# Optimization experiments

Measured on AMD Instinct MI355X. Metric: run time of the kernel, lower is better.

Reference implementation:

```python
import jax, jax.numpy as jnp
import numpy as np

# Central-difference gradients on a 5D field (b, d1, d2, d3, c); slices crop
# the two non-differentiated spatial axes by 1 on each side so all outputs align.

def grad_dx(f):
    return (f[:, 2:, 1:-1, 1:-1] - f[:, :-2, 1:-1, 1:-1]) * 0.5

def grad_dy(f):
    return (f[:, 1:-1, 2:, 1:-1] - f[:, 1:-1, :-2, 1:-1]) * 0.5

def grad_dz(f):
    return (f[:, 1:-1, 1:-1, 2:] - f[:, 1:-1, 1:-1, :-2]) * 0.5


def setup_inputs() -> dict:
    key = jax.random.key(0)
    ddf = jax.random.normal(key, (4, 160, 160, 160, 3), dtype=jnp.float32)
    return {"ddf": ddf}


def reference(ddf) -> jnp.ndarray:
    # first derivatives: (b, d-2, h-2, w-2, 3)
    dfdx = grad_dx(ddf)
    dfdy = grad_dy(ddf)
    dfdz = grad_dz(ddf)
    # second derivatives: (b, d-4, h-4, w-4, 3)
    dfdxx = grad_dx(dfdx)
    dfdyy = grad_dy(dfdy)
    dfdzz = grad_dz(dfdz)
    dfdxy = grad_dy(dfdx)
    dfdyz = grad_dz(dfdy)
    dfdxz = grad_dz(dfdx)
    energy = (dfdxx ** 2 + dfdyy ** 2 + dfdzz ** 2
              + 2.0 * dfdxy ** 2 + 2.0 * dfdxz ** 2 + 2.0 * dfdyz ** 2)
    return jnp.mean(energy, axis=(1, 2, 3, 4))  # shape (batch,)
```

## Files before the change

kernel.cpp:

```cpp
#include <hip/hip_runtime.h>


typedef float F4 __attribute__((ext_vector_type(4)));

#define DIM 160
#define SX (DIM * DIM * 3)
#define SY (DIM * 3)
#define FSZ ((long long)DIM * SX)
#define TOT (4LL * FSZ)

#define ROWS 20
#define ROWU 37
#define USED_U (ROWS * ROWU)
#define SLICE_U 744
#define SLICE_F (SLICE_U * 4)
#define SLOTS 4
#define STEPS 26
#define NSEG 6
#define NMS 4
#define NYT 10
#define NBLK (4 * NSEG * NMS * NYT)
#define CPX (NBLK / 8)

#define CB(a, i) a[(i) >> 2][(i) & 3]

__global__ __launch_bounds__(256, 2) void be_kernel(const float* __restrict__ f,
                                                    float* __restrict__ out) {
    __shared__ float lds[SLICE_F * SLOTS];
    const int tid = threadIdx.x;

    int lid = (blockIdx.x & 7) * CPX + (blockIdx.x >> 3);
    int p2i = lid / (NMS * NYT);
    int q2i = lid % (NMS * NYT);
    int b = p2i / NSEG, xseg = p2i % NSEG;
    int ms = q2i / NYT, yt = q2i % NYT;

    const int X0 = 2 + xseg * STEPS;
    const int gy0 = 16 * yt;
    const int core = 4 + 128 * ms;
    const int Gm = core - 8;
    const long long bb = (long long)b * FSZ;
    const float* fbase = f + bb;
    const float* fend = f + (TOT - 4);

    const int t = tid >> 4;
    const int yy = tid & 15;
    const int m0 = core + 8 * t;
    const int y = 2 + 16 * yt + yy;

    int jlo = 6 - m0; if (jlo < 0) jlo = 0;
    int jhi = 474 - m0; if (jhi > 8) jhi = 8;
    if (y >= DIM - 2) jhi = -1;

    const int rc = (yy + 2) * ROWU + 2 * t;

    long long choff[3];
#pragma unroll
    for (int it = 0; it < 3; ++it) {
        int c = it * 256 + tid;
        int row = c / ROWU, col = c - row * ROWU;
        choff[it] = (long long)(gy0 + row) * SY + Gm + 4 * col;
    }
    const bool ch2ok = (512 + tid) < USED_U;

    auto stage = [&](int slab, int slot) {
        long long sb = (long long)slab * SX;
#pragma unroll
        for (int it = 0; it < 3; ++it) {
            if (it < 2 || ch2ok) {
                const float* gp = fbase + (sb + choff[it]);
                gp = gp < f ? f : gp;
                gp = gp > fend ? fend : gp;
                __builtin_amdgcn_global_load_lds(
                    (const __attribute__((address_space(1))) unsigned int*)gp,
                    (__attribute__((address_space(3))) unsigned int*)
                        ((__attribute__((address_space(3))) float*)lds
                         + slot * SLICE_F + 4 * (it * 256 + tid)),
                    16, 0, 0);
            }
        }
    };

    auto LD = [&](const float* base, int unit) -> F4 {
        return *reinterpret_cast<const F4*>(base + 4 * unit);
    };

    stage(X0 - 2, 0); stage(X0 - 1, 1); stage(X0, 2); stage(X0 + 1, 3);
    __syncthreads();

    F4 r1[6], r2[4], r3[2];
    F4 p1[4], p2[2];
    F4 q1[4], q2[2];
    {
        const float* L2 = lds + 2 * SLICE_F;
        const float* L1 = lds + 1 * SLICE_F;
        const float* L0 = lds + 0 * SLICE_F;
#pragma unroll
        for (int i = 0; i < 6; ++i) r1[i] = LD(L2, rc + i);
#pragma unroll
        for (int i = 0; i < 4; ++i) r2[i] = LD(L1, rc + 1 + i);
        r3[0] = LD(L0, rc + 2); r3[1] = LD(L0, rc + 3);
#pragma unroll
        for (int i = 0; i < 4; ++i) {
            p1[i] = LD(L2, rc + ROWU + 1 + i);
            q1[i] = LD(L2, rc - ROWU + 1 + i);
        }
        p2[0] = LD(L1, rc + ROWU + 2); p2[1] = LD(L1, rc + ROWU + 3);
        q2[0] = LD(L1, rc - ROWU + 2); q2[1] = LD(L1, rc - ROWU + 3);
    }
    __syncthreads();
    stage(X0 + 2, 0);
    __syncthreads();

    float e = 0.0f;

    for (int s = 0; s < STEPS; ++s) {
        const int x = X0 + s;
        if (s <= STEPS - 2) stage(x + 3, (s + 1) & 3);

        const float* Lx  = lds + ((s + 2) & 3) * SLICE_F;
        const float* Lx1 = lds + ((s + 3) & 3) * SLICE_F;
        const float* Lx2 = lds + ((s) & 3) * SLICE_F;

        F4 r0[6], p0[4], q0[4], X2Pa[2], Y2Pa[2], Y2Ma[2];
#pragma unroll
        for (int i = 0; i < 6; ++i) r0[i] = LD(Lx1, rc + i);
#pragma unroll
        for (int i = 0; i < 4; ++i) {
            p0[i] = LD(Lx1, rc + ROWU + 1 + i);
            q0[i] = LD(Lx1, rc - ROWU + 1 + i);
        }
        X2Pa[0] = LD(Lx2, rc + 2);            X2Pa[1] = LD(Lx2, rc + 3);
        Y2Pa[0] = LD(Lx, rc + 2 * ROWU + 2);  Y2Pa[1] = LD(Lx, rc + 2 * ROWU + 3);
        Y2Ma[0] = LD(Lx, rc - 2 * ROWU + 2);  Y2Ma[1] = LD(Lx, rc - 2 * ROWU + 3);

#pragma unroll
        for (int j = 0; j < 8; ++j) {
            float ctr2 = 2.0f * CB(r1, j + 8);
            float dxx = (CB(X2Pa, j) + CB(r3, j)) - ctr2;
            float dyy = (CB(Y2Pa, j) + CB(Y2Ma, j)) - ctr2;
            float dzz = (CB(r1, j + 2) + CB(r1, j + 14)) - ctr2;
            float dxy = (CB(p0, j + 4) - CB(p2, j)) - (CB(q0, j + 4) - CB(q2, j));
            float dxz = (CB(r0, j + 11) - CB(r2, j + 7)) - (CB(r0, j + 5) - CB(r2, j + 1));
            float dyz = (CB(p1, j + 7) - CB(q1, j + 7)) - (CB(p1, j + 1) - CB(q1, j + 1));
            float dd = dxx * dxx + dyy * dyy + dzz * dzz;
            float dc = dxy * dxy + dxz * dxz + dyz * dyz;
            float msk = (j >= jlo && j < jhi) ? 1.0f : 0.0f;
            e += msk * (dd + 2.0f * dc);
        }

        r3[0] = r2[1]; r3[1] = r2[2];
#pragma unroll
        for (int i = 0; i < 4; ++i) r2[i] = r1[i + 1];
#pragma unroll
        for (int i = 0; i < 6; ++i) r1[i] = r0[i];
        p2[0] = p1[1]; p2[1] = p1[2];
        q2[0] = q1[1]; q2[1] = q1[2];
#pragma unroll
        for (int i = 0; i < 4; ++i) { p1[i] = p0[i]; q1[i] = q0[i]; }

        __syncthreads();
    }

#pragma unroll
    for (int off = 32; off > 0; off >>= 1) e += __shfl_down(e, off, 64);

    __shared__ float ws[4];
    int lane = tid & 63;
    int wid = tid >> 6;
    if (lane == 0) ws[wid] = e;
    __syncthreads();
    if (tid == 0) {
        const float inv_count = 0.0625f / (156.0f * 156.0f * 156.0f * 3.0f);
        atomicAdd(&out[b], (ws[0] + ws[1] + ws[2] + ws[3]) * inv_count);
    }
}

extern "C" void kernel_launch(void* const* d_in, const int* in_sizes, int n_in,
                              void* d_out, int out_size, void* d_ws, size_t ws_size,
                              hipStream_t stream) {
    const float* f = (const float*)d_in[0];
    float* out = (float*)d_out;

    hipMemsetAsync(d_out, 0, out_size * sizeof(float), stream);

    be_kernel<<<dim3(NBLK), dim3(256), 0, stream>>>(f, out);
}
```

Measured before the change: 92.59 us.

## Shrink register window, raise occupancy, and re-split x segments

Reworks the per-step register rolling window so only a few x-neighbor vectors are carried in registers, alternating two banks via a 2x-unrolled step lambda. Center-slice data and y-neighbors are re-read from LDS each step instead of being kept in registers. This cuts register pressure so launch bounds can be raised to 3 blocks per CU. It also shortens each block's x-march from 26 to 12 slabs with more segments, and permutes the thread-to-y mapping, which changes the LDS access pattern. The costs are more LDS reads per step and more halo restaging overhead per block.

```diff
diff --git a/kernel.cpp b/kernel.cpp
--- a/kernel.cpp
+++ b/kernel.cpp
@@ -15,8 +15,8 @@
 #define SLICE_U 744
 #define SLICE_F (SLICE_U * 4)
 #define SLOTS 4
-#define STEPS 26
-#define NSEG 6
+#define STEPS 12
+#define NSEG 13
 #define NMS 4
 #define NYT 10
 #define NBLK (4 * NSEG * NMS * NYT)
@@ -24,7 +24,7 @@
 
 #define CB(a, i) a[(i) >> 2][(i) & 3]
 
-__global__ __launch_bounds__(256, 2) void be_kernel(const float* __restrict__ f,
+__global__ __launch_bounds__(256, 3) void be_kernel(const float* __restrict__ f,
                                                     float* __restrict__ out) {
     __shared__ float lds[SLICE_F * SLOTS];
     const int tid = threadIdx.x;
@@ -44,7 +44,7 @@
     const float* fend = f + (TOT - 4);
 
     const int t = tid >> 4;
-    const int yy = tid & 15;
+    const int yy = ((tid >> 3) & 1) | ((tid & 7) << 1);
     const int m0 = core + 8 * t;
     const int y = 2 + 16 * yt + yy;
 
@@ -81,32 +81,28 @@
         }
     };
 
-    auto LD = [&](const float* base, int unit) -> F4 {
-        return *reinterpret_cast<const F4*>(base + 4 * unit);
-    };
-
     stage(X0 - 2, 0); stage(X0 - 1, 1); stage(X0, 2); stage(X0 + 1, 3);
     __syncthreads();
 
-    F4 r1[6], r2[4], r3[2];
-    F4 p1[4], p2[2];
-    F4 q1[4], q2[2];
+    F4 fa_xm[4], fa_pp[2], fa_pm[2], fb_xm[4], fb_pp[2], fb_pm[2], x2m[2];
     {
-        const float* L2 = lds + 2 * SLICE_F;
-        const float* L1 = lds + 1 * SLICE_F;
-        const float* L0 = lds + 0 * SLICE_F;
-#pragma unroll
-        for (int i = 0; i < 6; ++i) r1[i] = LD(L2, rc + i);
-#pragma unroll
-        for (int i = 0; i < 4; ++i) r2[i] = LD(L1, rc + 1 + i);
-        r3[0] = LD(L0, rc + 2); r3[1] = LD(L0, rc + 3);
+        const float* S1 = lds + 1 * SLICE_F;
+        const float* S2 = lds + 2 * SLICE_F;
+        const float* S0 = lds + 0 * SLICE_F;
 #pragma unroll
         for (int i = 0; i < 4; ++i) {
-            p1[i] = LD(L2, rc + ROWU + 1 + i);
-            q1[i] = LD(L2, rc - ROWU + 1 + i);
+            fa_xm[i] = *(const F4*)(S1 + 4 * (rc + 1 + i));
+            fb_xm[i] = *(const F4*)(S2 + 4 * (rc + 1 + i));
         }
-        p2[0] = LD(L1, rc + ROWU + 2); p2[1] = LD(L1, rc + ROWU + 3);
-        q2[0] = LD(L1, rc - ROWU + 2); q2[1] = LD(L1, rc - ROWU + 3);
+#pragma unroll
+        for (int i = 0; i < 2; ++i) {
+            fa_pp[i] = *(const F4*)(S1 + 4 * (rc + ROWU + 2 + i));
+            fa_pm[i] = *(const F4*)(S1 + 4 * (rc - ROWU + 2 + i));
+            fb_pp[i] = *(const F4*)(S2 + 4 * (rc + ROWU + 2 + i));
+            fb_pm[i] = *(const F4*)(S2 + 4 * (rc - ROWU + 2 + i));
+        }
+        x2m[0] = *(const F4*)(S0 + 4 * (rc + 2));
+        x2m[1] = *(const F4*)(S0 + 4 * (rc + 3));
     }
     __syncthreads();
     stage(X0 + 2, 0);
@@ -114,53 +110,66 @@
 
     float e = 0.0f;
 
-    for (int s = 0; s < STEPS; ++s) {
-        const int x = X0 + s;
-        if (s <= STEPS - 2) stage(x + 3, (s + 1) & 3);
+    auto step = [&](int s, bool do_stage, F4* Fxm, F4* Fpp, F4* Fpm) {
+        F4 sv0 = Fxm[1], sv1 = Fxm[2];
+        if (do_stage) stage(X0 + s + 3, (s + 1) & 3);
 
         const float* Lx  = lds + ((s + 2) & 3) * SLICE_F;
         const float* Lx1 = lds + ((s + 3) & 3) * SLICE_F;
         const float* Lx2 = lds + ((s) & 3) * SLICE_F;
 
-        F4 r0[6], p0[4], q0[4], X2Pa[2], Y2Pa[2], Y2Ma[2];
+        float C[24];
+        F4 XPn[4], PPn[2], PMn[2], YP4[4], YM4[4], X2Pa[2], Y2Pa[2], Y2Ma[2];
 #pragma unroll
-        for (int i = 0; i < 6; ++i) r0[i] = LD(Lx1, rc + i);
+        for (int i = 0; i < 6; ++i)
+            *(F4*)(&C[4 * i]) = *(const F4*)(Lx + 4 * (rc + i));
 #pragma unroll
         for (int i = 0; i < 4; ++i) {
-            p0[i] = LD(Lx1, rc + ROWU + 1 + i);
-            q0[i] = LD(Lx1, rc - ROWU + 1 + i);
+            XPn[i] = *(const F4*)(Lx1 + 4 * (rc + 1 + i));
+            YP4[i] = *(const F4*)(Lx + 4 * (rc + ROWU + 1 + i));
+            YM4[i] = *(const F4*)(Lx + 4 * (rc - ROWU + 1 + i));
         }
-        X2Pa[0] = LD(Lx2, rc + 2);            X2Pa[1] = LD(Lx2, rc + 3);
-        Y2Pa[0] = LD(Lx, rc + 2 * ROWU + 2);  Y2Pa[1] = LD(Lx, rc + 2 * ROWU + 3);
-        Y2Ma[0] = LD(Lx, rc - 2 * ROWU + 2);  Y2Ma[1] = LD(Lx, rc - 2 * ROWU + 3);
+#pragma unroll
+        for (int i = 0; i < 2; ++i) {
+            PPn[i]  = *(const F4*)(Lx1 + 4 * (rc + ROWU + 2 + i));
+            PMn[i]  = *(const F4*)(Lx1 + 4 * (rc - ROWU + 2 + i));
+            X2Pa[i] = *(const F4*)(Lx2 + 4 * (rc + 2 + i));
+            Y2Pa[i] = *(const F4*)(Lx + 4 * (rc + 2 * ROWU + 2 + i));
+            Y2Ma[i] = *(const F4*)(Lx + 4 * (rc - 2 * ROWU + 2 + i));
+        }
 
 #pragma unroll
         for (int j = 0; j < 8; ++j) {
-            float ctr2 = 2.0f * CB(r1, j + 8);
-            float dxx = (CB(X2Pa, j) + CB(r3, j)) - ctr2;
+            float ctr2 = 2.0f * C[j + 8];
+            float dxx = (CB(X2Pa, j) + CB(x2m, j)) - ctr2;
             float dyy = (CB(Y2Pa, j) + CB(Y2Ma, j)) - ctr2;
-            float dzz = (CB(r1, j + 2) + CB(r1, j + 14)) - ctr2;
-            float dxy = (CB(p0, j + 4) - CB(p2, j)) - (CB(q0, j + 4) - CB(q2, j));
-            float dxz = (CB(r0, j + 11) - CB(r2, j + 7)) - (CB(r0, j + 5) - CB(r2, j + 1));
-            float dyz = (CB(p1, j + 7) - CB(q1, j + 7)) - (CB(p1, j + 1) - CB(q1, j + 1));
+            float dzz = (C[j + 2] + C[j + 14]) - ctr2;
+            float dxy = (CB(PPn, j) - CB(Fpp, j)) - (CB(PMn, j) - CB(Fpm, j));
+            float dxz = (CB(XPn, j + 7) - CB(Fxm, j + 7))
+                      - (CB(XPn, j + 1) - CB(Fxm, j + 1));
+            float dyz = (CB(YP4, j + 7) - CB(YM4, j + 7))
+                      - (CB(YP4, j + 1) - CB(YM4, j + 1));
             float dd = dxx * dxx + dyy * dyy + dzz * dzz;
             float dc = dxy * dxy + dxz * dxz + dyz * dyz;
             float msk = (j >= jlo && j < jhi) ? 1.0f : 0.0f;
             e += msk * (dd + 2.0f * dc);
         }
 
-        r3[0] = r2[1]; r3[1] = r2[2];
 #pragma unroll
-        for (int i = 0; i < 4; ++i) r2[i] = r1[i + 1];
+        for (int i = 0; i < 4; ++i) Fxm[i] = XPn[i];
 #pragma unroll
-        for (int i = 0; i < 6; ++i) r1[i] = r0[i];
-        p2[0] = p1[1]; p2[1] = p1[2];
-        q2[0] = q1[1]; q2[1] = q1[2];
-#pragma unroll
-        for (int i = 0; i < 4; ++i) { p1[i] = p0[i]; q1[i] = q0[i]; }
+        for (int i = 0; i < 2; ++i) { Fpp[i] = PPn[i]; Fpm[i] = PMn[i]; }
+        x2m[0] = sv0; x2m[1] = sv1;
 
         __syncthreads();
+    };
+
+    for (int sp = 0; sp < 5; ++sp) {
+        step(2 * sp,     true, fa_xm, fa_pp, fa_pm);
+        step(2 * sp + 1, true, fb_xm, fb_pp, fb_pm);
     }
+    step(10, true,  fa_xm, fa_pp, fa_pm);
+    step(11, false, fb_xm, fb_pp, fb_pm);
 
 #pragma unroll
     for (int off = 32; off > 0; off >>= 1) e += __shfl_down(e, off, 64);
```

Result: slower. 150.1 us (+62.2%).
